# Kernel optimization log

Measured on AMD Instinct MI355X. Metric: run time of the kernel, lower is better.

Reference implementation:

```python
import jax, jax.numpy as jnp
import numpy as np

B = 32768
BACKCAST = 512
FORECAST = 96
UNITS = 512
THETAS = 32
NG = THETAS // 4  # gaussians
L = BACKCAST + FORECAST


def setup_inputs() -> dict:
    key = jax.random.key(0)
    ks = jax.random.split(key, 8)
    s = 0.02
    inp = {
        'x': jax.random.normal(ks[0], (B, BACKCAST), dtype=jnp.float32),
        'fc_w0': jax.random.normal(ks[1], (UNITS, BACKCAST), dtype=jnp.float32) * s,
        'fc_b0': jnp.zeros((UNITS,), jnp.float32),
        'fc_w1': jax.random.normal(ks[2], (UNITS, UNITS), dtype=jnp.float32) * s,
        'fc_b1': jnp.zeros((UNITS,), jnp.float32),
        'fc_w2': jax.random.normal(ks[3], (UNITS, UNITS), dtype=jnp.float32) * s,
        'fc_b2': jnp.zeros((UNITS,), jnp.float32),
        'fc_w3': jax.random.normal(ks[4], (UNITS, UNITS), dtype=jnp.float32) * s,
        'fc_b3': jnp.zeros((UNITS,), jnp.float32),
        'theta_w': jax.random.normal(ks[5], (THETAS, UNITS), dtype=jnp.float32) * s,
        'fn_g': jnp.ones((NG,), jnp.float32), 'fn_b': jnp.zeros((NG,), jnp.float32),
        'wn_g': jnp.ones((NG,), jnp.float32), 'wn_b': jnp.zeros((NG,), jnp.float32),
    }
    # fixed sinusoidal basis buffers
    freqs = (1.0 / np.arange(2.0, L * 2 + 1, dtype=np.float32))  # [2L-1]
    t_b = np.arange(BACKCAST, dtype=np.float32)
    t_f = np.arange(BACKCAST, BACKCAST + FORECAST, dtype=np.float32)
    arg_b = 2.0 * np.pi * freqs[:, None] * t_b
    arg_f = 2.0 * np.pi * freqs[:, None] * t_f
    inp['freqs'] = jnp.asarray(freqs)
    inp['s_backcast'] = jnp.asarray(np.concatenate([np.sin(arg_b), np.cos(arg_b)], 0))
    inp['s_forecast'] = jnp.asarray(np.concatenate([np.sin(arg_f), np.cos(arg_f)], 0))
    return inp


def _layernorm(v, g, b, eps=1e-5):
    m = jnp.mean(v, axis=-1, keepdims=True)
    var = jnp.mean(jnp.square(v - m), axis=-1, keepdims=True)
    return (v - m) * jax.lax.rsqrt(var + eps) * g + b


def _softplus10(v):
    # torch Softplus(beta=10)
    return jax.nn.softplus(10.0 * v) / 10.0


def reference(x, fc_w0, fc_b0, fc_w1, fc_b1, fc_w2, fc_b2, fc_w3, fc_b3,
              theta_w, fn_g, fn_b, wn_g, wn_b, freqs, s_backcast, s_forecast):
    # fc stack (dropout = identity in eval)
    h = jax.nn.relu(x @ fc_w0.T + fc_b0)
    h = jax.nn.relu(h @ fc_w1.T + fc_b1)
    h = jax.nn.relu(h @ fc_w2.T + fc_b2)
    h = jax.nn.relu(h @ fc_w3.T + fc_b3)
    coeff = h @ theta_w.T  # [B, THETAS]
    p = coeff.reshape(coeff.shape[0], -1, 4)  # [B, NG, 4]
    total_len = s_backcast.shape[1] + s_forecast.shape[1]
    cf = 1.0 / (1.0 + jax.nn.sigmoid(_layernorm(p[..., 3], fn_g, fn_b))[..., None] * total_len)  # [B,NG,1]
    inv_w = cf / jnp.maximum(_softplus10(_layernorm(p[..., 2], wn_g, wn_b))[..., None], 1e-6)
    exponent = jnp.square((freqs - cf) * inv_w) * 0.5  # [B, NG, F]
    norm_amp = jax.nn.softmax(exponent, axis=-1)
    amp_sin = jnp.sum(norm_amp * p[..., 0][..., None], axis=1)  # [B, F]
    amp_cos = jnp.sum(norm_amp * p[..., 1][..., None], axis=1)
    amps = jnp.concatenate([amp_sin, amp_cos], axis=-1)  # [B, 2F]
    backcast = amps @ s_backcast
    forecast = amps @ s_forecast
    return (backcast, forecast)
```

## Files before the change

kernel.cpp:

```cpp
#include <hip/hip_runtime.h>
#include <hip/hip_bf16.h>
#include <math.h>

#define BATCH 32768
#define UNITS 512
#define NF 1215
#define KF 2432
#define NOUT 608

typedef __bf16 bf16x8 __attribute__((ext_vector_type(8)));
typedef float f32x4 __attribute__((ext_vector_type(4)));
typedef short s16x4 __attribute__((ext_vector_type(4)));
typedef short s16x8 __attribute__((ext_vector_type(8)));

__device__ __forceinline__ unsigned short f2b(float f) {
  unsigned u = __builtin_bit_cast(unsigned, f);
  u += 0x7fffu + ((u >> 16) & 1u);
  return (unsigned short)(u >> 16);
}
__device__ __forceinline__ float b2f(unsigned short h) {
  unsigned u = ((unsigned)h) << 16;
  return __builtin_bit_cast(float, u);
}

#if __has_builtin(__builtin_amdgcn_exp2f)
__device__ __forceinline__ float fexp2(float x) { return __builtin_amdgcn_exp2f(x); }
#else
__device__ __forceinline__ float fexp2(float x) { return exp2f(x); }
#endif
#if __has_builtin(__builtin_amdgcn_logf)
__device__ __forceinline__ float flog2(float x) { return __builtin_amdgcn_logf(x); }
#else
__device__ __forceinline__ float flog2(float x) { return log2f(x); }
#endif
#if __has_builtin(__builtin_amdgcn_rcpf)
__device__ __forceinline__ float frcp(float x) { return __builtin_amdgcn_rcpf(x); }
#else
__device__ __forceinline__ float frcp(float x) { return 1.f / x; }
#endif

__device__ __forceinline__ void gload16(const unsigned short* g, unsigned short* l) {
  __builtin_amdgcn_global_load_lds(
      (const __attribute__((address_space(1))) void*)g,
      (__attribute__((address_space(3))) void*)l, 16, 0, 0);
}

template <int N> __device__ __forceinline__ void wait_vm() {
  if constexpr (N == 0)      asm volatile("s_waitcnt vmcnt(0)" ::: "memory");
  else if constexpr (N == 7) asm volatile("s_waitcnt vmcnt(7)" ::: "memory");
  else if constexpr (N == 8) asm volatile("s_waitcnt vmcnt(8)" ::: "memory");
  else                       asm volatile("s_waitcnt vmcnt(9)" ::: "memory");
}
__device__ __forceinline__ void barrier_raw() {
  asm volatile("" ::: "memory");
  __builtin_amdgcn_s_barrier();
  asm volatile("" ::: "memory");
}

__global__ __launch_bounds__(256) void split_k4(
    const float* __restrict__ src, unsigned short* __restrict__ hi,
    unsigned short* __restrict__ lo, int n4)
{
  int i = blockIdx.x * 256 + threadIdx.x;
  int stride = gridDim.x * 256;
  for (; i < n4; i += stride) {
    f32x4 v = ((const f32x4*)src)[i];
    s16x4 h, l;
#pragma unroll
    for (int j = 0; j < 4; ++j) {
      unsigned short hb = f2b(v[j]);
      h[j] = (short)hb;
      l[j] = (short)f2b(v[j] - b2f(hb));
    }
    ((s16x4*)hi)[i] = h;
    ((s16x4*)lo)[i] = l;
  }
}

__global__ __launch_bounds__(256) void st_prep(
    const float* __restrict__ sb, const float* __restrict__ sf,
    unsigned short* __restrict__ st)
{
  __shared__ float tile[32][33];
  int k0 = blockIdx.x * 32, n0 = blockIdx.y * 32;
  int tx = threadIdx.x, ty = threadIdx.y;
#pragma unroll
  for (int yy = 0; yy < 32; yy += 8) {
    int k = k0 + ty + yy, n = n0 + tx;
    float v = 0.f;
    if (k < 2430) {
      if (n < 512) v = sb[(size_t)k * 512 + n];
      else if (n < NOUT) v = sf[(size_t)k * 96 + (n - 512)];
    }
    tile[ty + yy][tx] = v;
  }
  __syncthreads();
#pragma unroll
  for (int yy = 0; yy < 32; yy += 8) {
    int n = n0 + ty + yy, k = k0 + tx;
    st[(size_t)n * KF + k] = f2b(tile[tx][ty + yy]);
  }
}

template <int NBN>
__global__ __launch_bounds__(256) void gemm_fc(
    const unsigned short* __restrict__ Agh, const unsigned short* __restrict__ Agl,
    const unsigned short* __restrict__ Bgh, const unsigned short* __restrict__ Bgl,
    const float* __restrict__ bias,
    unsigned short* __restrict__ Chi, unsigned short* __restrict__ Clo)
{
  constexpr int NT = 512 / 32;
  __shared__ unsigned short Ah[2][128 * 32];
  __shared__ unsigned short Bh[2][128 * 32];
  __shared__ unsigned short Al[2][128 * 32];
  __shared__ unsigned short Bl[2][128 * 32];

  const int t = threadIdx.x;
  const int lane = t & 63;
  const int w = t >> 6;
  const int wr = w >> 1, wc = w & 1;

  const int lin = blockIdx.x;
  const int xcd = lin & 7;
  const int sub = lin >> 3;
  const long bm = (long)(xcd * 32 + sub / NBN) * 128;
  const int bn = (sub % NBN) * 128;

  const int lr = lane & 15, kg = lane >> 4;

  const int Rw = lane >> 2;
  const int pch = lane & 3;
  const int R1 = w * 16 + Rw;
  const int R2 = (w + 4) * 16 + Rw;
  const int s1 = (pch - (R1 >> 1)) & 3;
  const int s2 = (pch - (R2 >> 1)) & 3;
  const size_t oA1 = (size_t)(bm + R1) * UNITS + s1 * 8;
  const size_t oA2 = (size_t)(bm + R2) * UNITS + s2 * 8;
  const size_t oB1 = (size_t)(bn + R1) * UNITS + s1 * 8;
  const size_t oB2 = (size_t)(bn + R2) * UNITS + s2 * 8;

  auto STAGE = [&](int buf, int kt) {
    gload16(Agh + oA1 + kt, &Ah[buf][w * 512]);
    gload16(Agh + oA2 + kt, &Ah[buf][(w + 4) * 512]);
    gload16(Bgh + oB1 + kt, &Bh[buf][w * 512]);
    gload16(Bgh + oB2 + kt, &Bh[buf][(w + 4) * 512]);
    gload16(Agl + oA1 + kt, &Al[buf][w * 512]);
    gload16(Agl + oA2 + kt, &Al[buf][(w + 4) * 512]);
    gload16(Bgl + oB1 + kt, &Bl[buf][w * 512]);
    gload16(Bgl + oB2 + kt, &Bl[buf][(w + 4) * 512]);
  };

  const f32x4 fzero = {0.f, 0.f, 0.f, 0.f};
  f32x4 acc[4][4];
#pragma unroll
  for (int m = 0; m < 4; ++m)
#pragma unroll
    for (int n = 0; n < 4; ++n) acc[m][n] = fzero;

  STAGE(0, 0);
  int cur = 0;
  for (int it = 0; it < NT; ++it) {
    if (it + 1 < NT) { STAGE(cur ^ 1, (it + 1) * 32); wait_vm<8>(); }
    else wait_vm<0>();
    barrier_raw();

    bf16x8 bhf[4], blf[4];
#pragma unroll
    for (int n = 0; n < 4; ++n) {
      int R = wc * 64 + n * 16 + lr;
      int phys = R * 32 + (((kg + (R >> 1)) & 3) << 3);
      bhf[n] = *(const bf16x8*)&Bh[cur][phys];
      blf[n] = *(const bf16x8*)&Bl[cur][phys];
    }
#pragma unroll
    for (int m = 0; m < 4; ++m) {
      int R = wr * 64 + m * 16 + lr;
      int phys = R * 32 + (((kg + (R >> 1)) & 3) << 3);
      bf16x8 ahf = *(const bf16x8*)&Ah[cur][phys];
      bf16x8 alf = *(const bf16x8*)&Al[cur][phys];
#pragma unroll
      for (int n = 0; n < 4; ++n) {
        acc[m][n] = __builtin_amdgcn_mfma_f32_16x16x32_bf16(ahf, bhf[n], acc[m][n], 0, 0, 0);
        acc[m][n] = __builtin_amdgcn_mfma_f32_16x16x32_bf16(ahf, blf[n], acc[m][n], 0, 0, 0);
        acc[m][n] = __builtin_amdgcn_mfma_f32_16x16x32_bf16(alf, bhf[n], acc[m][n], 0, 0, 0);
      }
    }
    barrier_raw();
    cur ^= 1;
  }

#pragma unroll
  for (int m = 0; m < 4; ++m) {
#pragma unroll
    for (int n = 0; n < 4; ++n) {
      long gr0 = bm + wr * 64 + m * 16 + kg * 4;
      int gc = bn + wc * 64 + n * 16 + lr;
      float bv = bias[gc];
#pragma unroll
      for (int r = 0; r < 4; ++r) {
        float o = fmaxf(acc[m][n][r] + bv, 0.f);
        unsigned short h = f2b(o);
        size_t off = (size_t)(gr0 + r) * UNITS + gc;
        Chi[off] = h;
        Clo[off] = f2b(o - b2f(h));
      }
    }
  }
}

__global__ __launch_bounds__(256, 2) void gemm_wide(
    const unsigned short* __restrict__ Ag, const unsigned short* __restrict__ Bg,
    float* __restrict__ outF)
{
  constexpr int NT = KF / 32;
  __shared__ unsigned short Ah[3][128 * 32];
  __shared__ unsigned short Bh[2][320 * 32];

  const int t = threadIdx.x;
  const int lane = t & 63;
  const int w = t >> 6;
  const int wr = w >> 1, wc = w & 1;

  const int lin = blockIdx.x;
  const int xcd = lin & 7;
  const int sub = lin >> 3;
  const long bm = (long)(xcd * 32 + (sub >> 1)) * 128;
  const int bn = (sub & 1) * 320;

  const int lr = lane & 15, kg = lane >> 4;
  const int Rl = lane >> 2, pch = lane & 3;

  const int RA1 = w * 16 + Rl, RA2 = (w + 4) * 16 + Rl;
  const int sA1 = (pch - (RA1 >> 1)) & 3, sA2 = (pch - (RA2 >> 1)) & 3;
  const size_t oA1 = (size_t)(bm + RA1) * KF + sA1 * 8;
  const size_t oA2 = (size_t)(bm + RA2) * KF + sA2 * 8;
  size_t oB[5];
#pragma unroll
  for (int j = 0; j < 5; ++j) {
    int q = w * 5 + j;
    int R = q * 16 + Rl;
    int s = (pch - (R >> 1)) & 3;
    oB[j] = (size_t)(bn + R) * KF + s * 8;
  }

  auto STAGE_A = [&](int buf, int kt) {
    gload16(Ag + oA1 + kt, &Ah[buf][w * 512]);
    gload16(Ag + oA2 + kt, &Ah[buf][(w + 4) * 512]);
  };
  auto STAGE_B = [&](int buf, int kt) {
#pragma unroll
    for (int j = 0; j < 5; ++j)
      gload16(Bg + oB[j] + kt, &Bh[buf][(w * 5 + j) * 512]);
  };

  const f32x4 fzero = {0.f, 0.f, 0.f, 0.f};
  f32x4 acc[4][10];
#pragma unroll
  for (int m = 0; m < 4; ++m)
#pragma unroll
    for (int n = 0; n < 10; ++n) acc[m][n] = fzero;

  STAGE_A(0, 0);
  STAGE_B(0, 0);
  STAGE_A(1, 32);

  int ia = 0;
  int ib = 0;
  for (int k = 0; k < NT; ++k) {
    if (k + 1 < NT) STAGE_B(ib ^ 1, (k + 1) * 32);
    if (k + 2 < NT) STAGE_A(ia >= 1 ? ia - 1 : 2, (k + 2) * 32);
    if (k < NT - 2)      wait_vm<9>();
    else if (k == NT - 2) wait_vm<7>();
    else                  wait_vm<0>();
    barrier_raw();

    bf16x8 af[4];
#pragma unroll
    for (int m = 0; m < 4; ++m) {
      int R = wr * 64 + m * 16 + lr;
      af[m] = *(const bf16x8*)&Ah[ia][R * 32 + (((kg + (R >> 1)) & 3) << 3)];
    }
#pragma unroll
    for (int n = 0; n < 10; ++n) {
      int R = wc * 160 + n * 16 + lr;
      bf16x8 bf = *(const bf16x8*)&Bh[ib][R * 32 + (((kg + (R >> 1)) & 3) << 3)];
#pragma unroll
      for (int m = 0; m < 4; ++m)
        acc[m][n] = __builtin_amdgcn_mfma_f32_16x16x32_bf16(af[m], bf, acc[m][n], 0, 0, 0);
    }
    barrier_raw();
    ia = (ia + 1 == 3) ? 0 : ia + 1;
    ib ^= 1;
  }

#pragma unroll
  for (int m = 0; m < 4; ++m) {
#pragma unroll
    for (int n = 0; n < 10; ++n) {
      long gr0 = bm + wr * 64 + m * 16 + kg * 4;
      int gc = bn + wc * 160 + n * 16 + lr;
      if (gc < NOUT) {
#pragma unroll
        for (int r = 0; r < 4; ++r) {
          float o = acc[m][n][r];
          long row = gr0 + r;
          if (gc < 512) outF[row * 512 + gc] = o;
          else outF[(size_t)BATCH * 512 + row * 96 + (gc - 512)] = o;
        }
      }
    }
  }
}

__global__ __launch_bounds__(256) void coeff_gemm(
    const unsigned short* __restrict__ Agh, const unsigned short* __restrict__ Agl,
    const unsigned short* __restrict__ Bgh, const unsigned short* __restrict__ Bgl,
    float* __restrict__ coeff)
{
  __shared__ unsigned short Ah[128 * 32];
  __shared__ unsigned short Al[128 * 32];
  __shared__ unsigned short Bh[32 * 32];
  __shared__ unsigned short Bl[32 * 32];

  const int t = threadIdx.x;
  const int lane = t & 63;
  const int w = t >> 6;
  const long bm = (long)blockIdx.x * 128;
  const int lr = lane & 15, kg = lane >> 4;

  const f32x4 fzero = {0.f, 0.f, 0.f, 0.f};
  f32x4 acc[2][2];
#pragma unroll
  for (int m = 0; m < 2; ++m)
#pragma unroll
    for (int n = 0; n < 2; ++n) acc[m][n] = fzero;

  for (int kt = 0; kt < 512; kt += 32) {
    __syncthreads();
#pragma unroll
    for (int p = 0; p < 2; ++p) {
      int c = t + 256 * p;
      int row = c >> 2, slot = c & 3;
      int phys = row * 32 + (((slot + (row >> 1)) & 3) << 3);
      size_t go = (size_t)(bm + row) * UNITS + kt + slot * 8;
      *(s16x8*)&Ah[phys] = *(const s16x8*)&Agh[go];
      *(s16x8*)&Al[phys] = *(const s16x8*)&Agl[go];
    }
    if (t < 128) {
      int row = t >> 2, slot = t & 3;
      int phys = row * 32 + (((slot + (row >> 1)) & 3) << 3);
      size_t go = (size_t)row * UNITS + kt + slot * 8;
      *(s16x8*)&Bh[phys] = *(const s16x8*)&Bgh[go];
      *(s16x8*)&Bl[phys] = *(const s16x8*)&Bgl[go];
    }
    __syncthreads();

    bf16x8 bh[2], bl[2];
#pragma unroll
    for (int n = 0; n < 2; ++n) {
      int R = n * 16 + lr;
      int phys = R * 32 + (((kg + (R >> 1)) & 3) << 3);
      bh[n] = *(const bf16x8*)&Bh[phys];
      bl[n] = *(const bf16x8*)&Bl[phys];
    }
#pragma unroll
    for (int m = 0; m < 2; ++m) {
      int R = w * 32 + m * 16 + lr;
      int phys = R * 32 + (((kg + (R >> 1)) & 3) << 3);
      bf16x8 ah = *(const bf16x8*)&Ah[phys];
      bf16x8 al = *(const bf16x8*)&Al[phys];
#pragma unroll
      for (int n = 0; n < 2; ++n) {
        acc[m][n] = __builtin_amdgcn_mfma_f32_16x16x32_bf16(ah, bh[n], acc[m][n], 0, 0, 0);
        acc[m][n] = __builtin_amdgcn_mfma_f32_16x16x32_bf16(ah, bl[n], acc[m][n], 0, 0, 0);
        acc[m][n] = __builtin_amdgcn_mfma_f32_16x16x32_bf16(al, bh[n], acc[m][n], 0, 0, 0);
      }
    }
  }
#pragma unroll
  for (int m = 0; m < 2; ++m)
#pragma unroll
    for (int n = 0; n < 2; ++n) {
      long gr0 = bm + w * 32 + m * 16 + kg * 4;
      int gc = n * 16 + lr;
#pragma unroll
      for (int r = 0; r < 4; ++r)
        coeff[(size_t)(gr0 + r) * 32 + gc] = acc[m][n][r];
    }
}

__global__ __launch_bounds__(256, 1) void gauss_kernel(
    const float* __restrict__ coeff, const float* __restrict__ fn_g,
    const float* __restrict__ fn_b, const float* __restrict__ wn_g,
    const float* __restrict__ wn_b, const float* __restrict__ freqs,
    unsigned short* __restrict__ amps)
{
  const int wid = threadIdx.x >> 6;
  const int t = threadIdx.x & 63;
  const int b = blockIdx.x * 4 + wid;
  const float cv = coeff[(size_t)b * 32 + (t & 31)];
  const float L2E = 1.4426950408889634f;

  float c2[8], c3[8];
  float m2 = 0.f, m3 = 0.f;
#pragma unroll
  for (int g = 0; g < 8; ++g) {
    c2[g] = __shfl(cv, 4 * g + 2);
    c3[g] = __shfl(cv, 4 * g + 3);
    m2 += c2[g]; m3 += c3[g];
  }
  m2 *= 0.125f; m3 *= 0.125f;
  float v2 = 0.f, v3 = 0.f;
#pragma unroll
  for (int g = 0; g < 8; ++g) {
    float d2 = c2[g] - m2; v2 += d2 * d2;
    float d3 = c3[g] - m3; v3 += d3 * d3;
  }
  v2 *= 0.125f; v3 *= 0.125f;
  const float r2 = rsqrtf(v2 + 1e-5f), r3 = rsqrtf(v3 + 1e-5f);

  const float S2 = 0.8493218f;
  const float fv0 = freqs[0], fvL = freqs[NF - 1];
  float aa[8], oo[8], mxm[8];
#pragma unroll
  for (int g = 0; g < 8; ++g) {
    float z3 = (c3[g] - m3) * r3 * fn_g[g] + fn_b[g];
    float sig = frcp(1.f + fexp2(-z3 * L2E));
    float cfg = frcp(1.f + sig * 608.f);
    float z2 = (c2[g] - m2) * r2 * wn_g[g] + wn_b[g];
    float x = 10.f * z2;
    float enx = fexp2(-fabsf(x) * L2E);
    float sp = (fmaxf(x, 0.f) + 0.6931471805599453f * flog2(1.f + enx)) * 0.1f;
    float iwg = cfg * frcp(fmaxf(sp, 1e-6f));
    aa[g] = iwg * S2;
    oo[g] = cfg * iwg * S2;
    float d0 = fmaf(fv0, aa[g], -oo[g]);
    float dL = fmaf(fvL, aa[g], -oo[g]);
    mxm[g] = fmaxf(d0 * d0, dL * dL);
  }

  float sm[8];
#pragma unroll
  for (int g = 0; g < 8; ++g) sm[g] = 0.f;

  unsigned pk[19][4];
#pragma unroll
  for (int i = 0; i < 19; ++i) {
    int f = t + 64 * i;
    float fv = freqs[min(f, NF - 1)];
#pragma unroll
    for (int j = 0; j < 4; ++j) {
      float d0 = fmaf(fv, aa[2 * j], -oo[2 * j]);
      float e0 = fexp2(fmaf(d0, d0, -mxm[2 * j]));
      float d1 = fmaf(fv, aa[2 * j + 1], -oo[2 * j + 1]);
      float e1 = fexp2(fmaf(d1, d1, -mxm[2 * j + 1]));
      if (i == 18 && t == 63) { e0 = 0.f; e1 = 0.f; }
      unsigned b0 = __builtin_bit_cast(unsigned, e0) & 0xFFFF0000u;
      unsigned b1 = __builtin_bit_cast(unsigned, e1) & 0xFFFF0000u;
      unsigned pw = b1 | (b0 >> 16);
      asm volatile("" : "+v"(pw));
      pk[i][j] = pw;
      sm[2 * j]     += __builtin_bit_cast(float, b0);
      sm[2 * j + 1] += __builtin_bit_cast(float, b1);
    }
  }

  float wsn[8], wcn[8];
#pragma unroll
  for (int g = 0; g < 8; ++g) {
#pragma unroll
    for (int m = 32; m >= 1; m >>= 1) sm[g] += __shfl_xor(sm[g], m);
    float inv = frcp(sm[g]);
    wsn[g] = __shfl(cv, 4 * g + 0) * inv;
    wcn[g] = __shfl(cv, 4 * g + 1) * inv;
  }

  size_t base = (size_t)b * KF;
#pragma unroll
  for (int i = 0; i < 19; ++i) {
    float as = 0.f, ac = 0.f;
#pragma unroll
    for (int j = 0; j < 4; ++j) {
      unsigned pw = pk[i][j];
      float e0 = __builtin_bit_cast(float, pw << 16);
      float e1 = __builtin_bit_cast(float, pw & 0xFFFF0000u);
      as = fmaf(e0, wsn[2 * j], as);
      as = fmaf(e1, wsn[2 * j + 1], as);
      ac = fmaf(e0, wcn[2 * j], ac);
      ac = fmaf(e1, wcn[2 * j + 1], ac);
    }
    int f = t + 64 * i;
    if (f < NF) {
      amps[base + f] = f2b(as);
      amps[base + NF + f] = f2b(ac);
    }
  }
  if (t == 0) {
    amps[base + 2430] = 0;
    amps[base + 2431] = 0;
  }
}

extern "C" void kernel_launch(void* const* d_in, const int* in_sizes, int n_in,
                              void* d_out, int out_size, void* d_ws, size_t ws_size,
                              hipStream_t stream) {
  (void)in_sizes; (void)n_in; (void)out_size; (void)ws_size;
  const float* x = (const float*)d_in[0];
  const float* fcw[4] = {(const float*)d_in[1], (const float*)d_in[3],
                         (const float*)d_in[5], (const float*)d_in[7]};
  const float* fcb[4] = {(const float*)d_in[2], (const float*)d_in[4],
                         (const float*)d_in[6], (const float*)d_in[8]};
  const float* theta_w = (const float*)d_in[9];
  const float* fn_g = (const float*)d_in[10];
  const float* fn_b = (const float*)d_in[11];
  const float* wn_g = (const float*)d_in[12];
  const float* wn_b = (const float*)d_in[13];
  const float* freqs = (const float*)d_in[14];
  const float* sb = (const float*)d_in[15];
  const float* sf = (const float*)d_in[16];
  float* out = (float*)d_out;

  char* p = (char*)d_ws;
  auto take = [&](size_t bytes) {
    char* r = p;
    p += (bytes + 255) & ~(size_t)255;
    return r;
  };
  unsigned short* h0h = (unsigned short*)take((size_t)BATCH * UNITS * 2);
  unsigned short* h0l = (unsigned short*)take((size_t)BATCH * UNITS * 2);
  unsigned short* h1h = (unsigned short*)take((size_t)BATCH * UNITS * 2);
  unsigned short* h1l = (unsigned short*)take((size_t)BATCH * UNITS * 2);
  unsigned short *wh[4], *wl[4];
  for (int l = 0; l < 4; ++l) {
    wh[l] = (unsigned short*)take((size_t)UNITS * UNITS * 2);
    wl[l] = (unsigned short*)take((size_t)UNITS * UNITS * 2);
  }
  unsigned short* twh = (unsigned short*)take((size_t)32 * UNITS * 2);
  unsigned short* twl = (unsigned short*)take((size_t)32 * UNITS * 2);
  float* coeff = (float*)take((size_t)BATCH * 32 * 4);
  unsigned short* st = (unsigned short*)take((size_t)640 * KF * 2);
  unsigned short* amps = (unsigned short*)take((size_t)BATCH * KF * 2);

  split_k4<<<2048, 256, 0, stream>>>(x, h0h, h0l, BATCH * UNITS / 4);
  for (int l = 0; l < 4; ++l)
    split_k4<<<256, 256, 0, stream>>>(fcw[l], wh[l], wl[l], UNITS * UNITS / 4);
  split_k4<<<16, 256, 0, stream>>>(theta_w, twh, twl, 32 * UNITS / 4);
  st_prep<<<dim3(KF / 32, 640 / 32), dim3(32, 8), 0, stream>>>(sb, sf, st);

  gemm_fc<4><<<4 * (BATCH / 128), 256, 0, stream>>>(
      h0h, h0l, wh[0], wl[0], fcb[0], h1h, h1l);
  gemm_fc<4><<<4 * (BATCH / 128), 256, 0, stream>>>(
      h1h, h1l, wh[1], wl[1], fcb[1], h0h, h0l);
  gemm_fc<4><<<4 * (BATCH / 128), 256, 0, stream>>>(
      h0h, h0l, wh[2], wl[2], fcb[2], h1h, h1l);
  gemm_fc<4><<<4 * (BATCH / 128), 256, 0, stream>>>(
      h1h, h1l, wh[3], wl[3], fcb[3], h0h, h0l);

  coeff_gemm<<<BATCH / 128, 256, 0, stream>>>(h0h, h0l, twh, twl, coeff);

  gauss_kernel<<<BATCH / 4, 256, 0, stream>>>(coeff, fn_g, fn_b, wn_g, wn_b, freqs, amps);

  gemm_wide<<<2 * (BATCH / 128), 256, 0, stream>>>(amps, st, out);
}
```

Measured before the change: 505.8 us.

## Load GEMM A operand directly into registers and simplify bf16 packing

```diff
diff --git a/kernel.cpp b/kernel.cpp
--- a/kernel.cpp
+++ b/kernel.cpp
@@ -47,7 +47,6 @@
 
 template <int N> __device__ __forceinline__ void wait_vm() {
   if constexpr (N == 0)      asm volatile("s_waitcnt vmcnt(0)" ::: "memory");
-  else if constexpr (N == 7) asm volatile("s_waitcnt vmcnt(7)" ::: "memory");
   else if constexpr (N == 8) asm volatile("s_waitcnt vmcnt(8)" ::: "memory");
   else                       asm volatile("s_waitcnt vmcnt(9)" ::: "memory");
 }
@@ -213,7 +212,6 @@
     float* __restrict__ outF)
 {
   constexpr int NT = KF / 32;
-  __shared__ unsigned short Ah[3][128 * 32];
   __shared__ unsigned short Bh[2][320 * 32];
 
   const int t = threadIdx.x;
@@ -230,10 +228,6 @@
   const int lr = lane & 15, kg = lane >> 4;
   const int Rl = lane >> 2, pch = lane & 3;
 
-  const int RA1 = w * 16 + Rl, RA2 = (w + 4) * 16 + Rl;
-  const int sA1 = (pch - (RA1 >> 1)) & 3, sA2 = (pch - (RA2 >> 1)) & 3;
-  const size_t oA1 = (size_t)(bm + RA1) * KF + sA1 * 8;
-  const size_t oA2 = (size_t)(bm + RA2) * KF + sA2 * 8;
   size_t oB[5];
 #pragma unroll
   for (int j = 0; j < 5; ++j) {
@@ -242,17 +236,19 @@
     int s = (pch - (R >> 1)) & 3;
     oB[j] = (size_t)(bn + R) * KF + s * 8;
   }
-
-  auto STAGE_A = [&](int buf, int kt) {
-    gload16(Ag + oA1 + kt, &Ah[buf][w * 512]);
-    gload16(Ag + oA2 + kt, &Ah[buf][(w + 4) * 512]);
-  };
   auto STAGE_B = [&](int buf, int kt) {
 #pragma unroll
     for (int j = 0; j < 5; ++j)
       gload16(Bg + oB[j] + kt, &Bh[buf][(w * 5 + j) * 512]);
   };
 
+  const unsigned short* aPtr = Ag + (size_t)(bm + wr * 64 + lr) * KF + kg * 8;
+  auto LOAD_A = [&](bf16x8 (&dst)[4], int kt) {
+#pragma unroll
+    for (int m = 0; m < 4; ++m)
+      dst[m] = *(const bf16x8*)(aPtr + (size_t)m * 16 * KF + kt);
+  };
+
   const f32x4 fzero = {0.f, 0.f, 0.f, 0.f};
   f32x4 acc[4][10];
 #pragma unroll
@@ -260,37 +256,35 @@
 #pragma unroll
     for (int n = 0; n < 10; ++n) acc[m][n] = fzero;
 
-  STAGE_A(0, 0);
+  bf16x8 aA[4], aB[4];
   STAGE_B(0, 0);
-  STAGE_A(1, 32);
-
-  int ia = 0;
+  LOAD_A(aA, 0);
+
   int ib = 0;
-  for (int k = 0; k < NT; ++k) {
-    if (k + 1 < NT) STAGE_B(ib ^ 1, (k + 1) * 32);
-    if (k + 2 < NT) STAGE_A(ia >= 1 ? ia - 1 : 2, (k + 2) * 32);
-    if (k < NT - 2)      wait_vm<9>();
-    else if (k == NT - 2) wait_vm<7>();
-    else                  wait_vm<0>();
+  auto ITER = [&](bf16x8 (&acur)[4], bf16x8 (&anext)[4], int k) {
+    if (k + 1 < NT) {
+      STAGE_B(ib ^ 1, (k + 1) * 32);
+      LOAD_A(anext, (k + 1) * 32);
+      wait_vm<9>();
+    } else {
+      wait_vm<0>();
+    }
     barrier_raw();
 
-    bf16x8 af[4];
-#pragma unroll
-    for (int m = 0; m < 4; ++m) {
-      int R = wr * 64 + m * 16 + lr;
-      af[m] = *(const bf16x8*)&Ah[ia][R * 32 + (((kg + (R >> 1)) & 3) << 3)];
-    }
 #pragma unroll
     for (int n = 0; n < 10; ++n) {
       int R = wc * 160 + n * 16 + lr;
       bf16x8 bf = *(const bf16x8*)&Bh[ib][R * 32 + (((kg + (R >> 1)) & 3) << 3)];
 #pragma unroll
       for (int m = 0; m < 4; ++m)
-        acc[m][n] = __builtin_amdgcn_mfma_f32_16x16x32_bf16(af[m], bf, acc[m][n], 0, 0, 0);
+        acc[m][n] = __builtin_amdgcn_mfma_f32_16x16x32_bf16(acur[m], bf, acc[m][n], 0, 0, 0);
     }
     barrier_raw();
-    ia = (ia + 1 == 3) ? 0 : ia + 1;
     ib ^= 1;
+  };
+  for (int k = 0; k < NT; k += 2) {
+    ITER(aA, aB, k);
+    ITER(aB, aA, k + 1);
   }
 
 #pragma unroll
@@ -455,13 +449,13 @@
       float d1 = fmaf(fv, aa[2 * j + 1], -oo[2 * j + 1]);
       float e1 = fexp2(fmaf(d1, d1, -mxm[2 * j + 1]));
       if (i == 18 && t == 63) { e0 = 0.f; e1 = 0.f; }
-      unsigned b0 = __builtin_bit_cast(unsigned, e0) & 0xFFFF0000u;
-      unsigned b1 = __builtin_bit_cast(unsigned, e1) & 0xFFFF0000u;
-      unsigned pw = b1 | (b0 >> 16);
+      unsigned pw = __builtin_amdgcn_perm(__builtin_bit_cast(unsigned, e1),
+                                          __builtin_bit_cast(unsigned, e0),
+                                          0x07060302u);
       asm volatile("" : "+v"(pw));
       pk[i][j] = pw;
-      sm[2 * j]     += __builtin_bit_cast(float, b0);
-      sm[2 * j + 1] += __builtin_bit_cast(float, b1);
+      sm[2 * j]     += e0;
+      sm[2 * j + 1] += e1;
     }
   }
 
```

Result: slower. 535.4 us (+5.8%).
